# Optimization experiments

Measured on AMD Instinct MI355X. Metric: run time of the kernel, lower is better.

The kernel has to match this reference:

```python
import jax, jax.numpy as jnp
import numpy as np

B = 256        # graph pairs
MAX_SET = 64   # nodes per graph == max_set_size (padding is identity)
E = 512        # edges per graph
D = 128        # node_state_dim == av.filters_3
T = 64         # av.transform_dim
N_PROP = 5
N_TIME = 3
TEMP = 0.1
SINK_ITERS = 20
NG = 2 * B
N = NG * MAX_SET
TOT_E = NG * E


def sinkhorn(log_alpha):
    la = log_alpha / TEMP
    for _ in range(SINK_ITERS):
        la = la - jax.nn.logsumexp(la, axis=2, keepdims=True)
        la = la - jax.nn.logsumexp(la, axis=1, keepdims=True)
    return jnp.exp(la)


def setup_inputs() -> dict:
    key = jax.random.key(0)
    ks = jax.random.split(key, 32)

    def lin(k, i, o):
        return jax.random.normal(k, (i, o), jnp.float32) / np.sqrt(i).astype(np.float32)

    node_features = jax.random.normal(ks[0], (N, 32), jnp.float32)
    edge_features = jax.random.normal(ks[1], (TOT_E, 16), jnp.float32)
    offs = jnp.repeat(jnp.arange(NG, dtype=jnp.int32) * MAX_SET, E)
    from_idx = jax.random.randint(ks[2], (TOT_E,), 0, MAX_SET, jnp.int32) + offs
    to_idx = jax.random.randint(ks[3], (TOT_E,), 0, MAX_SET, jnp.int32) + offs
    return {
        "node_features": node_features, "edge_features": edge_features,
        "from_idx": from_idx, "to_idx": to_idx,
        "node_enc_w": lin(ks[4], 32, D), "node_enc_b": jnp.zeros((D,), jnp.float32),
        "edge_enc_w": lin(ks[5], 16, 64), "edge_enc_b": jnp.zeros((64,), jnp.float32),
        "mw1": lin(ks[6], 2 * D + 64, 2 * D), "mb1": jnp.zeros((2 * D,), jnp.float32),
        "mw2": lin(ks[7], 2 * D, D), "mb2": jnp.zeros((D,), jnp.float32),
        "nw1": lin(ks[8], 2 * D, 2 * D), "nb1": jnp.zeros((2 * D,), jnp.float32),
        "nw2": lin(ks[9], 2 * D, D), "nb2": jnp.zeros((D,), jnp.float32),
        "cw1": lin(ks[10], 2 * D, 2 * D), "cb1": jnp.zeros((2 * D,), jnp.float32),
        "cw2": lin(ks[11], 2 * D, D), "cb2": jnp.zeros((D,), jnp.float32),
        "t1w": lin(ks[12], D, T), "t1b": jnp.zeros((T,), jnp.float32),
        "t2w": lin(ks[13], T, T), "t2b": jnp.zeros((T,), jnp.float32),
    }


def reference(node_features, edge_features, from_idx, to_idx,
              node_enc_w, node_enc_b, edge_enc_w, edge_enc_b,
              mw1, mb1, mw2, mb2, nw1, nb1, nw2, nb2,
              cw1, cb1, cw2, cb2, t1w, t1b, t2w, t2b):
    # Encoder (GMN GraphEncoder: linear maps on raw node/edge features)
    h0 = node_features @ node_enc_w + node_enc_b          # [N, D]
    e0 = edge_features @ edge_enc_w + edge_enc_b          # [TOT_E, 64]
    store = jnp.zeros((N, D * (N_PROP + 1)), h0.dtype)    # node_feature_store
    plan = None
    for _t in range(N_TIME):
        h = h0
        parts = [jnp.zeros((N, D), h0.dtype)]             # slot 0 stays zero
        for p in range(1, N_PROP + 1):
            inter = store[:, (p - 1) * D: p * D]          # time_update_idx == 'k_t'
            comb = jax.nn.relu(jnp.concatenate([h, inter], 1) @ cw1 + cb1) @ cw2 + cb2
            # GraphPropLayer: gather -> message MLP -> segment_sum -> node update MLP
            msg_in = jnp.concatenate([comb[from_idx], comb[to_idx], e0], 1)
            messages = jax.nn.relu(msg_in @ mw1 + mb1) @ mw2 + mb2
            agg = jax.ops.segment_sum(messages, to_idx, num_segments=N)
            h = jax.nn.relu(jnp.concatenate([comb, agg], 1) @ nw1 + nb1) @ nw2 + nb2
            parts.append(h)
        store = jnp.concatenate(parts, 1)                 # [N, D*(K+1)]
        # split into padded query/corpus stacks (all graphs have MAX_SET nodes,
        # so F.pad and the size masks are identity here)
        s = store.reshape(NG, MAX_SET, -1)
        q, c = s[0::2], s[1::2]                           # [B, M, D*(K+1)]
        tq = jax.nn.relu(q[:, :, -D:] @ t1w + t1b) @ t2w + t2b
        tc = jax.nn.relu(c[:, :, -D:] @ t1w + t1b) @ t2w + t2b
        sim = jnp.einsum('bqt,bct->bqc', tq, tc)
        plan = sinkhorn(sim)                              # node transport plan [B,M,M]
        qfc = jnp.einsum('bqc,bcd->bqd', plan, c)
        cfq = jnp.einsum('bqc,bqd->bcd', plan, q)
        inter_feats = jnp.stack([qfc, cfq], 1)[:, :, :, D:].reshape(N, N_PROP * D)
        store = store.at[:, D:].set(inter_feats)
    return plan
```

## Files before the change

### kernel.cpp

```cpp
#include <hip/hip_runtime.h>
#include <hip/hip_bf16.h>

#define NNODES   32768
#define NGROUPS  512
#define EPG      512
#define ND       (32768l*128)

typedef __attribute__((ext_vector_type(4))) float f32x4;
typedef __attribute__((ext_vector_type(8))) short bf16x8;

__device__ __forceinline__ short f2bf(float x) {
  unsigned u = __float_as_uint(x);
  unsigned r = (u + 0x7FFF + ((u >> 16) & 1)) >> 16;
  return (short)r;
}
__device__ __forceinline__ float bf2f(short h) {
  return __uint_as_float(((unsigned)(unsigned short)h) << 16);
}
__device__ __forceinline__ void split3(float x, short* ph, short* pm, short* pl, long idx) {
  short h = f2bf(x); float r1 = x - bf2f(h);
  short m = f2bf(r1); float r2 = r1 - bf2f(m);
  ph[idx] = h; pm[idx] = m; pl[idx] = f2bf(r2);
}

__global__ void k_node_enc(const float* __restrict__ nf, const float* __restrict__ w,
                           const float* __restrict__ b, float* __restrict__ h0) {
  int idx = blockIdx.x * 256 + threadIdx.x;
  int row = idx >> 7, col = idx & 127;
  const float* x = nf + row * 32;
  float acc = b[col];
#pragma unroll
  for (int k = 0; k < 32; ++k) acc = fmaf(x[k], w[k * 128 + col], acc);
  h0[idx] = acc;
}

__global__ void k_prep(const float* __restrict__ eew, const float* __restrict__ eeb,
                       const float* __restrict__ mw1, const float* __restrict__ mb1,
                       const float* __restrict__ mb2, const float* __restrict__ nw1,
                       float* __restrict__ Wfold, float* __restrict__ bfold,
                       float* __restrict__ vbias) {
  const int c = threadIdx.x, b = blockIdx.x;
  if (b < 16) {
    float a = 0.f;
    for (int j = 0; j < 64; ++j) a = fmaf(eew[b * 64 + j], mw1[(256 + j) * 256 + c], a);
    Wfold[b * 256 + c] = a;
  } else if (b == 16) {
    float a = mb1[c];
    for (int j = 0; j < 64; ++j) a = fmaf(eeb[j], mw1[(256 + j) * 256 + c], a);
    bfold[c] = a;
  } else {
    float a = 0.f;
    for (int j = 0; j < 128; ++j) a = fmaf(mb2[j], nw1[(128 + j) * 256 + c], a);
    vbias[c] = a;
  }
}

__global__ void k_wsplit3(const float* __restrict__ W, int C, int Kd,
                          short* __restrict__ th, short* __restrict__ tm,
                          short* __restrict__ tl) {
  const int c = blockIdx.x;
  for (int k = threadIdx.x; k < Kd; k += 256) {
    float w = W[(long)k * C + c];
    split3(w, th, tm, tl, c * 256 + k);
  }
}

__global__ void k_csr(const int* __restrict__ from_idx, const int* __restrict__ to_idx,
                      const float* __restrict__ ef,
                      int* __restrict__ csr_f, int* __restrict__ rp_g,
                      float* __restrict__ efp, int* __restrict__ deg) {
  __shared__ int cnt[64], rps[65];
  __shared__ int tls[EPG], fls[EPG];
  __shared__ short ord[EPG];
  const int g = blockIdx.x, tid = threadIdx.x;
  const int be = g * EPG, bn = g * 64;
  if (tid < 64) cnt[tid] = 0;
  __syncthreads();
  for (int e = tid; e < EPG; e += 256) {
    int t = to_idx[be + e] - bn;
    tls[e] = t;
    fls[e] = from_idx[be + e] - bn;
    atomicAdd(&cnt[t], 1);
  }
  __syncthreads();
  if (tid == 0) {
    int s = 0;
    for (int i = 0; i < 64; ++i) { rps[i] = s; s += cnt[i]; }
    rps[64] = s;
  }
  __syncthreads();
  if (tid < 64) {
    int pos = rps[tid];
    for (int e = 0; e < EPG; ++e)
      if (tls[e] == tid) ord[pos++] = (short)e;
  }
  __syncthreads();
  for (int ec = tid; ec < EPG; ec += 256) {
    const int eo = ord[ec];
    csr_f[be + ec] = fls[eo];
    const float4* src = (const float4*)&ef[(long)(be + eo) * 16];
    float4* dst = (float4*)&efp[(long)(be + ec) * 16];
    dst[0] = src[0]; dst[1] = src[1]; dst[2] = src[2]; dst[3] = src[3];
  }
  if (tid < 65) rp_g[g * 65 + tid] = rps[tid];
  if (tid < 64) deg[bn + tid] = cnt[tid];
}

template<int KTOT, bool DEG, bool RPX0, bool WPOUT, bool AGG>
__global__ __launch_bounds__(256, 3)
void k_mlp2m(const float* __restrict__ x0,
             const short* __restrict__ x0h, const short* __restrict__ x0m,
             const short* __restrict__ x0l,
             const float* __restrict__ x1,
             const short* __restrict__ A2h, const short* __restrict__ A2m,
             const short* __restrict__ A2l,
             const short* __restrict__ W1h, const short* __restrict__ W1m,
             const short* __restrict__ W1l,
             const float* __restrict__ b1, const int* __restrict__ deg,
             const float* __restrict__ vbias,
             const short* __restrict__ W2h, const short* __restrict__ W2m,
             const short* __restrict__ W2l,
             const float* __restrict__ b2,
             float* __restrict__ out,
             short* __restrict__ outh, short* __restrict__ outm,
             short* __restrict__ outl) {
  __shared__ short xh[32 * 264];
  __shared__ short xm[32 * 264];
  __shared__ short xl[32 * 264];
  __shared__ int degs[32];
  const int tid = threadIdx.x;
  const long row0 = (long)blockIdx.x * 32;

  const int lane = tid & 63, wid = tid >> 6;
  const int lr = lane & 15;
  const int lk = (lane >> 4) * 8;
  const int rsub = (lane >> 4) * 4;

  if constexpr (AGG) {
    for (int i = tid; i < 2048; i += 256) {
      const int r = i >> 6, q = i & 63;
      float4 v = *(const float4*)&x1[(row0 + r) * 256 + q * 4];
      const int base = r * 264 + q * 4;
      split3(v.x, xh, xm, xl, base + 0);
      split3(v.y, xh, xm, xl, base + 1);
      split3(v.z, xh, xm, xl, base + 2);
      split3(v.w, xh, xm, xl, base + 3);
    }
    __syncthreads();

    f32x4 s0[2][2], s1[2][2];
#pragma unroll
    for (int fc = 0; fc < 2; ++fc)
#pragma unroll
      for (int fr = 0; fr < 2; ++fr) { s0[fr][fc] = {0.f,0.f,0.f,0.f}; s1[fr][fc] = {0.f,0.f,0.f,0.f}; }

#pragma unroll 2
    for (int ks = 0; ks < 4; ++ks) {
      const int k0 = ks * 32 + lk;
      bf16x8 ah[2], am[2], al[2];
#pragma unroll
      for (int fr = 0; fr < 2; ++fr) {
        const int ab = (fr * 16 + lr) * 264 + k0;
        ah[fr] = *(const bf16x8*)&xh[ab];
        am[fr] = *(const bf16x8*)&xm[ab];
        al[fr] = *(const bf16x8*)&xl[ab];
      }
#pragma unroll
      for (int fc = 0; fc < 2; ++fc) {
        const long wrow = (long)(wid * 32 + fc * 16 + lr) * 256 + k0;
        const bf16x8 bh = *(const bf16x8*)&A2h[wrow];
        const bf16x8 bm = *(const bf16x8*)&A2m[wrow];
        const bf16x8 bl = *(const bf16x8*)&A2l[wrow];
#pragma unroll
        for (int fr = 0; fr < 2; ++fr) {
          s0[fr][fc] = __builtin_amdgcn_mfma_f32_16x16x32_bf16(ah[fr], bh, s0[fr][fc], 0, 0, 0);
          s0[fr][fc] = __builtin_amdgcn_mfma_f32_16x16x32_bf16(ah[fr], bm, s0[fr][fc], 0, 0, 0);
          s0[fr][fc] = __builtin_amdgcn_mfma_f32_16x16x32_bf16(am[fr], bh, s0[fr][fc], 0, 0, 0);
          s0[fr][fc] = __builtin_amdgcn_mfma_f32_16x16x32_bf16(ah[fr], bl, s0[fr][fc], 0, 0, 0);
          s0[fr][fc] = __builtin_amdgcn_mfma_f32_16x16x32_bf16(am[fr], bm, s0[fr][fc], 0, 0, 0);
          s0[fr][fc] = __builtin_amdgcn_mfma_f32_16x16x32_bf16(al[fr], bh, s0[fr][fc], 0, 0, 0);
        }
      }
    }
#pragma unroll 2
    for (int ks = 4; ks < 8; ++ks) {
      const int k0 = ks * 32 + lk;
      bf16x8 ah[2], am[2], al[2];
#pragma unroll
      for (int fr = 0; fr < 2; ++fr) {
        const int ab = (fr * 16 + lr) * 264 + k0;
        ah[fr] = *(const bf16x8*)&xh[ab];
        am[fr] = *(const bf16x8*)&xm[ab];
        al[fr] = *(const bf16x8*)&xl[ab];
      }
#pragma unroll
      for (int fc = 0; fc < 2; ++fc) {
        const long wrow = (long)(wid * 32 + fc * 16 + lr) * 256 + k0;
        const bf16x8 bh = *(const bf16x8*)&A2h[wrow];
        const bf16x8 bm = *(const bf16x8*)&A2m[wrow];
        const bf16x8 bl = *(const bf16x8*)&A2l[wrow];
#pragma unroll
        for (int fr = 0; fr < 2; ++fr) {
          s1[fr][fc] = __builtin_amdgcn_mfma_f32_16x16x32_bf16(ah[fr], bh, s1[fr][fc], 0, 0, 0);
          s1[fr][fc] = __builtin_amdgcn_mfma_f32_16x16x32_bf16(ah[fr], bm, s1[fr][fc], 0, 0, 0);
          s1[fr][fc] = __builtin_amdgcn_mfma_f32_16x16x32_bf16(am[fr], bh, s1[fr][fc], 0, 0, 0);
          s1[fr][fc] = __builtin_amdgcn_mfma_f32_16x16x32_bf16(ah[fr], bl, s1[fr][fc], 0, 0, 0);
          s1[fr][fc] = __builtin_amdgcn_mfma_f32_16x16x32_bf16(am[fr], bm, s1[fr][fc], 0, 0, 0);
          s1[fr][fc] = __builtin_amdgcn_mfma_f32_16x16x32_bf16(al[fr], bh, s1[fr][fc], 0, 0, 0);
        }
      }
    }
    __syncthreads();

#pragma unroll
    for (int fr = 0; fr < 2; ++fr)
#pragma unroll
      for (int fc = 0; fc < 2; ++fc) {
        const int col = wid * 32 + fc * 16 + lr;
#pragma unroll
        for (int r = 0; r < 4; ++r) {
          const int row = fr * 16 + rsub + r;
          split3(s0[fr][fc][r] + s1[fr][fc][r], xh, xm, xl, row * 264 + 128 + col);
        }
      }
  }

  if constexpr (RPX0) {
    for (int i = tid; i < 32 * 16; i += 256) {
      const int r = i >> 4, q = i & 15;
      const long gb = (row0 + r) * 128 + q * 8;
      const int lb = r * 264 + q * 8;
      *(bf16x8*)&xh[lb] = *(const bf16x8*)&x0h[gb];
      *(bf16x8*)&xm[lb] = *(const bf16x8*)&x0m[gb];
      *(bf16x8*)&xl[lb] = *(const bf16x8*)&x0l[gb];
    }
  } else {
    for (int i = tid; i < 32 * 32; i += 256) {
      const int r = i >> 5, q = i & 31;
      float4 v = *(const float4*)&x0[(row0 + r) * 128 + q * 4];
      const int base = r * 264 + q * 4;
      split3(v.x, xh, xm, xl, base + 0);
      split3(v.y, xh, xm, xl, base + 1);
      split3(v.z, xh, xm, xl, base + 2);
      split3(v.w, xh, xm, xl, base + 3);
    }
  }
  if constexpr (KTOT == 256 && !AGG) {
    for (int i = tid; i < 32 * 32; i += 256) {
      const int r = i >> 5, q = i & 31;
      float4 v = *(const float4*)&x1[(row0 + r) * 128 + q * 4];
      const int base = r * 264 + 128 + q * 4;
      split3(v.x, xh, xm, xl, base + 0);
      split3(v.y, xh, xm, xl, base + 1);
      split3(v.z, xh, xm, xl, base + 2);
      split3(v.w, xh, xm, xl, base + 3);
    }
  }
  if constexpr (DEG) { if (tid < 32) degs[tid] = deg[row0 + tid]; }
  __syncthreads();

  f32x4 acc[2][4];
#pragma unroll
  for (int fc = 0; fc < 4; ++fc) {
    const int col = wid * 64 + fc * 16 + lr;
    const float bv = b1[col];
#pragma unroll
    for (int fr = 0; fr < 2; ++fr) acc[fr][fc] = {bv, bv, bv, bv};
    if constexpr (DEG) {
      const float vb = vbias[col];
#pragma unroll
      for (int fr = 0; fr < 2; ++fr)
#pragma unroll
        for (int r = 0; r < 4; ++r)
          acc[fr][fc][r] += (float)degs[fr * 16 + rsub + r] * vb;
    }
  }

#pragma unroll 2
  for (int ks = 0; ks < KTOT / 32; ++ks) {
    const int k0 = ks * 32 + lk;
    bf16x8 ah[2], am[2], al[2];
#pragma unroll
    for (int fr = 0; fr < 2; ++fr) {
      const int ab = (fr * 16 + lr) * 264 + k0;
      ah[fr] = *(const bf16x8*)&xh[ab];
      am[fr] = *(const bf16x8*)&xm[ab];
      al[fr] = *(const bf16x8*)&xl[ab];
    }
#pragma unroll
    for (int fc = 0; fc < 4; ++fc) {
      const long wrow = (long)(wid * 64 + fc * 16 + lr) * 256 + k0;
      const bf16x8 bh = *(const bf16x8*)&W1h[wrow];
      const bf16x8 bm = *(const bf16x8*)&W1m[wrow];
      const bf16x8 bl = *(const bf16x8*)&W1l[wrow];
#pragma unroll
      for (int fr = 0; fr < 2; ++fr) {
        acc[fr][fc] = __builtin_amdgcn_mfma_f32_16x16x32_bf16(ah[fr], bh, acc[fr][fc], 0, 0, 0);
        acc[fr][fc] = __builtin_amdgcn_mfma_f32_16x16x32_bf16(ah[fr], bm, acc[fr][fc], 0, 0, 0);
        acc[fr][fc] = __builtin_amdgcn_mfma_f32_16x16x32_bf16(am[fr], bh, acc[fr][fc], 0, 0, 0);
        acc[fr][fc] = __builtin_amdgcn_mfma_f32_16x16x32_bf16(ah[fr], bl, acc[fr][fc], 0, 0, 0);
        acc[fr][fc] = __builtin_amdgcn_mfma_f32_16x16x32_bf16(am[fr], bm, acc[fr][fc], 0, 0, 0);
        acc[fr][fc] = __builtin_amdgcn_mfma_f32_16x16x32_bf16(al[fr], bh, acc[fr][fc], 0, 0, 0);
      }
    }
  }
  __syncthreads();

#pragma unroll
  for (int fr = 0; fr < 2; ++fr)
#pragma unroll
    for (int fc = 0; fc < 4; ++fc) {
      const int col = wid * 64 + fc * 16 + lr;
#pragma unroll
      for (int r = 0; r < 4; ++r) {
        const int row = fr * 16 + rsub + r;
        float v = fmaxf(acc[fr][fc][r], 0.f);
        split3(v, xh, xm, xl, row * 264 + col);
      }
    }
  __syncthreads();

  f32x4 acc2[2][2];
#pragma unroll
  for (int fc = 0; fc < 2; ++fc) {
    const float bv = b2[wid * 32 + fc * 16 + lr];
#pragma unroll
    for (int fr = 0; fr < 2; ++fr) acc2[fr][fc] = {bv, bv, bv, bv};
  }
#pragma unroll 2
  for (int ks = 0; ks < 8; ++ks) {
    const int k0 = ks * 32 + lk;
    bf16x8 ah[2], am[2], al[2];
#pragma unroll
    for (int fr = 0; fr < 2; ++fr) {
      const int ab = (fr * 16 + lr) * 264 + k0;
      ah[fr] = *(const bf16x8*)&xh[ab];
      am[fr] = *(const bf16x8*)&xm[ab];
      al[fr] = *(const bf16x8*)&xl[ab];
    }
#pragma unroll
    for (int fc = 0; fc < 2; ++fc) {
      const long wrow = (long)(wid * 32 + fc * 16 + lr) * 256 + k0;
      const bf16x8 bh = *(const bf16x8*)&W2h[wrow];
      const bf16x8 bm = *(const bf16x8*)&W2m[wrow];
      const bf16x8 bl = *(const bf16x8*)&W2l[wrow];
#pragma unroll
      for (int fr = 0; fr < 2; ++fr) {
        acc2[fr][fc] = __builtin_amdgcn_mfma_f32_16x16x32_bf16(ah[fr], bh, acc2[fr][fc], 0, 0, 0);
        acc2[fr][fc] = __builtin_amdgcn_mfma_f32_16x16x32_bf16(ah[fr], bm, acc2[fr][fc], 0, 0, 0);
        acc2[fr][fc] = __builtin_amdgcn_mfma_f32_16x16x32_bf16(am[fr], bh, acc2[fr][fc], 0, 0, 0);
        acc2[fr][fc] = __builtin_amdgcn_mfma_f32_16x16x32_bf16(ah[fr], bl, acc2[fr][fc], 0, 0, 0);
        acc2[fr][fc] = __builtin_amdgcn_mfma_f32_16x16x32_bf16(am[fr], bm, acc2[fr][fc], 0, 0, 0);
        acc2[fr][fc] = __builtin_amdgcn_mfma_f32_16x16x32_bf16(al[fr], bh, acc2[fr][fc], 0, 0, 0);
      }
    }
  }
#pragma unroll
  for (int fr = 0; fr < 2; ++fr)
#pragma unroll
    for (int fc = 0; fc < 2; ++fc) {
      const int col = wid * 32 + fc * 16 + lr;
#pragma unroll
      for (int r = 0; r < 4; ++r) {
        const long gi = (row0 + fr * 16 + rsub + r) * 128 + col;
        if constexpr (WPOUT) {
          split3(acc2[fr][fc][r], outh, outm, outl, gi);
        } else {
          out[gi] = acc2[fr][fc][r];
        }
      }
    }
}

__global__ __launch_bounds__(256, 3)
void k_edgeb(const short* __restrict__ chp, const short* __restrict__ cmp,
             const short* __restrict__ clp,
             const float* __restrict__ efp,
             const short* __restrict__ m1h, const short* __restrict__ m1m,
             const short* __restrict__ m1l,
             const float* __restrict__ Wfold, const float* __restrict__ bfold,
             const int* __restrict__ csr_f, const int* __restrict__ rp_g,
             float* __restrict__ ag) {
  __shared__ __align__(16) float cAB[2 * 64 * 68];
  __shared__ short fl[EPG];
  __shared__ int rp[65];
  float* cA = cAB;
  float* cB = cAB + 64 * 68;

  const int tid = threadIdx.x;
  const int g = blockIdx.x, cb = blockIdx.y;
  const int be = g * EPG, bn = g * 64;
  const int col0 = cb * 64;

  for (int i = tid; i < EPG; i += 256) fl[i] = (short)csr_f[be + i];
  if (tid < 65) rp[tid] = rp_g[g * 65 + tid];

  const int lane = tid & 63, wid = tid >> 6;
  const int lr = lane & 15;
  const int lk = (lane >> 4) * 8;
  const int rsub = (lane >> 4) * 4;
  const int ng = tid >> 4, cg = tid & 15;
  const int n0 = ng * 4, cq = cg * 4;

  {
    const int isB = wid >> 1;
    const int cw = (wid & 1) * 32;
    const int wkof = isB * 128;
    float* dstC = isB ? cB : cA;
#pragma unroll 1
    for (int hf = 0; hf < 2; ++hf) {
      f32x4 c[2][2];
#pragma unroll
      for (int fr = 0; fr < 2; ++fr)
#pragma unroll
        for (int fc = 0; fc < 2; ++fc) c[fr][fc] = {0.f, 0.f, 0.f, 0.f};
      for (int ks = 0; ks < 4; ++ks) {
        const int k0 = ks * 32 + lk;
        bf16x8 ah[2], am[2], al[2];
#pragma unroll
        for (int fr = 0; fr < 2; ++fr) {
          const long ga = (long)(bn + (hf * 2 + fr) * 16 + lr) * 128 + k0;
          ah[fr] = *(const bf16x8*)&chp[ga];
          am[fr] = *(const bf16x8*)&cmp[ga];
          al[fr] = *(const bf16x8*)&clp[ga];
        }
#pragma unroll
        for (int fc = 0; fc < 2; ++fc) {
          const long wrow = (long)(col0 + cw + fc * 16 + lr) * 256 + wkof + k0;
          const bf16x8 bh = *(const bf16x8*)&m1h[wrow];
          const bf16x8 bm = *(const bf16x8*)&m1m[wrow];
          const bf16x8 bl = *(const bf16x8*)&m1l[wrow];
#pragma unroll
          for (int fr = 0; fr < 2; ++fr) {
            c[fr][fc] = __builtin_amdgcn_mfma_f32_16x16x32_bf16(ah[fr], bh, c[fr][fc], 0, 0, 0);
            c[fr][fc] = __builtin_amdgcn_mfma_f32_16x16x32_bf16(ah[fr], bm, c[fr][fc], 0, 0, 0);
            c[fr][fc] = __builtin_amdgcn_mfma_f32_16x16x32_bf16(am[fr], bh, c[fr][fc], 0, 0, 0);
            c[fr][fc] = __builtin_amdgcn_mfma_f32_16x16x32_bf16(ah[fr], bl, c[fr][fc], 0, 0, 0);
            c[fr][fc] = __builtin_amdgcn_mfma_f32_16x16x32_bf16(am[fr], bm, c[fr][fc], 0, 0, 0);
            c[fr][fc] = __builtin_amdgcn_mfma_f32_16x16x32_bf16(al[fr], bh, c[fr][fc], 0, 0, 0);
          }
        }
      }
#pragma unroll
      for (int fr = 0; fr < 2; ++fr)
#pragma unroll
        for (int fc = 0; fc < 2; ++fc) {
          const int col = cw + fc * 16 + lr;
#pragma unroll
          for (int r = 0; r < 4; ++r)
            dstC[((hf * 2 + fr) * 16 + rsub + r) * 68 + col] = c[fr][fc][r];
        }
    }
  }
  float4 Wf[16];
#pragma unroll
  for (int k = 0; k < 16; ++k) Wf[k] = *(const float4*)&Wfold[k * 256 + col0 + cq];
  const float4 bf = *(const float4*)&bfold[col0 + cq];
  __syncthreads();

#pragma unroll
  for (int i = 0; i < 4; ++i) {
    const int n = n0 + i;
    const float4 cBn = *(const float4*)&cB[n * 68 + cq];
    const int eEnd = rp[n + 1];
    float4 a0 = make_float4(0.f, 0.f, 0.f, 0.f);
    float4 a1 = make_float4(0.f, 0.f, 0.f, 0.f);
    float4 a2 = make_float4(0.f, 0.f, 0.f, 0.f);
    int e = rp[n];
    for (; e + 2 < eEnd; e += 3) {
      const int f0 = fl[e], f1 = fl[e + 1], f2 = fl[e + 2];
      const float* er0 = efp + (long)(be + e) * 16;
      const float* er1 = efp + (long)(be + e + 1) * 16;
      const float* er2 = efp + (long)(be + e + 2) * 16;
      float4 ea[4], eb[4], ec[4];
#pragma unroll
      for (int kq = 0; kq < 4; ++kq) {
        ea[kq] = ((const float4*)er0)[kq];
        eb[kq] = ((const float4*)er1)[kq];
        ec[kq] = ((const float4*)er2)[kq];
      }
      float4 h0 = bf, h1 = bf, h2 = bf;
#pragma unroll
      for (int kq = 0; kq < 4; ++kq) {
        const float ev0[4] = {ea[kq].x, ea[kq].y, ea[kq].z, ea[kq].w};
        const float ev1[4] = {eb[kq].x, eb[kq].y, eb[kq].z, eb[kq].w};
        const float ev2[4] = {ec[kq].x, ec[kq].y, ec[kq].z, ec[kq].w};
#pragma unroll
        for (int s = 0; s < 4; ++s) {
          const float4 w = Wf[kq * 4 + s];
          h0.x = fmaf(ev0[s], w.x, h0.x); h0.y = fmaf(ev0[s], w.y, h0.y);
          h0.z = fmaf(ev0[s], w.z, h0.z); h0.w = fmaf(ev0[s], w.w, h0.w);
          h1.x = fmaf(ev1[s], w.x, h1.x); h1.y = fmaf(ev1[s], w.y, h1.y);
          h1.z = fmaf(ev1[s], w.z, h1.z); h1.w = fmaf(ev1[s], w.w, h1.w);
          h2.x = fmaf(ev2[s], w.x, h2.x); h2.y = fmaf(ev2[s], w.y, h2.y);
          h2.z = fmaf(ev2[s], w.z, h2.z); h2.w = fmaf(ev2[s], w.w, h2.w);
        }
      }
      const float4 va0 = *(const float4*)&cA[f0 * 68 + cq];
      const float4 va1 = *(const float4*)&cA[f1 * 68 + cq];
      const float4 va2 = *(const float4*)&cA[f2 * 68 + cq];
      a0.x += fmaxf(h0.x + va0.x + cBn.x, 0.f);
      a0.y += fmaxf(h0.y + va0.y + cBn.y, 0.f);
      a0.z += fmaxf(h0.z + va0.z + cBn.z, 0.f);
      a0.w += fmaxf(h0.w + va0.w + cBn.w, 0.f);
      a1.x += fmaxf(h1.x + va1.x + cBn.x, 0.f);
      a1.y += fmaxf(h1.y + va1.y + cBn.y, 0.f);
      a1.z += fmaxf(h1.z + va1.z + cBn.z, 0.f);
      a1.w += fmaxf(h1.w + va1.w + cBn.w, 0.f);
      a2.x += fmaxf(h2.x + va2.x + cBn.x, 0.f);
      a2.y += fmaxf(h2.y + va2.y + cBn.y, 0.f);
      a2.z += fmaxf(h2.z + va2.z + cBn.z, 0.f);
      a2.w += fmaxf(h2.w + va2.w + cBn.w, 0.f);
    }
    for (; e < eEnd; ++e) {
      const int f = fl[e];
      const float* er = efp + (long)(be + e) * 16;
      float4 h = bf;
#pragma unroll
      for (int kq = 0; kq < 4; ++kq) {
        const float4 e4 = ((const float4*)er)[kq];
        const float ev[4] = {e4.x, e4.y, e4.z, e4.w};
#pragma unroll
        for (int s = 0; s < 4; ++s) {
          const float4 w = Wf[kq * 4 + s];
          h.x = fmaf(ev[s], w.x, h.x); h.y = fmaf(ev[s], w.y, h.y);
          h.z = fmaf(ev[s], w.z, h.z); h.w = fmaf(ev[s], w.w, h.w);
        }
      }
      const float4 va = *(const float4*)&cA[f * 68 + cq];
      a0.x += fmaxf(h.x + va.x + cBn.x, 0.f);
      a0.y += fmaxf(h.y + va.y + cBn.y, 0.f);
      a0.z += fmaxf(h.z + va.z + cBn.z, 0.f);
      a0.w += fmaxf(h.w + va.w + cBn.w, 0.f);
    }
    a0.x += a1.x; a0.y += a1.y; a0.z += a1.z; a0.w += a1.w;
    a0.x += a2.x; a0.y += a2.y; a0.z += a2.z; a0.w += a2.w;
    *(float4*)&ag[(long)(bn + n) * 256 + col0 + cq] = a0;
  }
}

__global__ void k_tfeat(const float* __restrict__ x,
                        const float* __restrict__ t1w, const float* __restrict__ t1b,
                        const float* __restrict__ t2w, const float* __restrict__ t2b,
                        float* __restrict__ tf) {
  __shared__ float xs[4][128];
  __shared__ float ys[4][64];
  const int tid = threadIdx.x;
  const long row0 = (long)blockIdx.x * 4;
  for (int i = tid; i < 512; i += 256)
    xs[i >> 7][i & 127] = x[(row0 + (i >> 7)) * 128 + (i & 127)];
  __syncthreads();
  const int r = tid >> 6, c = tid & 63;
  float acc = t1b[c];
#pragma unroll 4
  for (int k = 0; k < 128; ++k) acc = fmaf(xs[r][k], t1w[k * 64 + c], acc);
  ys[r][c] = fmaxf(acc, 0.f);
  __syncthreads();
  float a2 = t2b[c];
#pragma unroll 4
  for (int k = 0; k < 64; ++k) a2 = fmaf(ys[r][k], t2w[k * 64 + c], a2);
  tf[(row0 + r) * 64 + c] = a2;
}

__global__ void k_sim(const float* __restrict__ tf, float* __restrict__ sim) {
  const int b = blockIdx.x, tid = threadIdx.x;
  __shared__ float tq[64][65];
  __shared__ float tcs[64][65];
  for (int i = tid; i < 4096; i += 256) {
    tq[i >> 6][i & 63]  = tf[(long)b * 8192 + i];
    tcs[i >> 6][i & 63] = tf[(long)b * 8192 + 4096 + i];
  }
  __syncthreads();
  const int m = tid >> 2, j0 = (tid & 3) * 16;
#pragma unroll
  for (int j = 0; j < 16; ++j) {
    float a = 0.f;
#pragma unroll 4
    for (int k = 0; k < 64; ++k) a = fmaf(tq[m][k], tcs[j0 + j][k], a);
    sim[(long)b * 4096 + m * 64 + j0 + j] = a;
  }
}

__global__ void k_sink(float* __restrict__ sim, float* __restrict__ outp) {
  const int b = blockIdx.x, tid = threadIdx.x;
  __shared__ float la[64][65];
  const float C = 14.426950408889634f;
  for (int i = tid; i < 4096; i += 256)
    la[i >> 6][i & 63] = sim[(long)b * 4096 + i] * C;
  __syncthreads();
  const int r4 = tid >> 2, l4 = tid & 3;
  for (int it = 0; it < 20; ++it) {
    {
      float m = -3.4e38f;
#pragma unroll
      for (int i = 0; i < 16; ++i) m = fmaxf(m, la[r4][l4 + 4 * i]);
      m = fmaxf(m, __shfl_xor(m, 1)); m = fmaxf(m, __shfl_xor(m, 2));
      float s = 0.f;
#pragma unroll
      for (int i = 0; i < 16; ++i) s += exp2f(la[r4][l4 + 4 * i] - m);
      s += __shfl_xor(s, 1); s += __shfl_xor(s, 2);
      const float lse = m + log2f(s);
#pragma unroll
      for (int i = 0; i < 16; ++i) la[r4][l4 + 4 * i] -= lse;
    }
    __syncthreads();
    {
      float m = -3.4e38f;
#pragma unroll
      for (int i = 0; i < 16; ++i) m = fmaxf(m, la[l4 + 4 * i][r4]);
      m = fmaxf(m, __shfl_xor(m, 1)); m = fmaxf(m, __shfl_xor(m, 2));
      float s = 0.f;
#pragma unroll
      for (int i = 0; i < 16; ++i) s += exp2f(la[l4 + 4 * i][r4] - m);
      s += __shfl_xor(s, 1); s += __shfl_xor(s, 2);
      const float lse = m + log2f(s);
#pragma unroll
      for (int i = 0; i < 16; ++i) la[l4 + 4 * i][r4] -= lse;
    }
    __syncthreads();
  }
  for (int i = tid; i < 4096; i += 256) {
    const float v = exp2f(la[i >> 6][i & 63]);
    outp[(long)b * 4096 + i] = v;
    sim[(long)b * 4096 + i] = v;
  }
}

__global__ void k_mix(const float* __restrict__ plan, const float* __restrict__ src,
                      float* __restrict__ dst) {
  const int b = blockIdx.x, tid = threadIdx.x;
  __shared__ float pl[64][65];
  __shared__ float qs[64][128];
  __shared__ float cs[64][128];
  const long qbase = (long)(2 * b) * 64, cbase = qbase + 64;
  for (int i = tid; i < 4096; i += 256) pl[i >> 6][i & 63] = plan[(long)b * 4096 + i];
  for (int i = tid; i < 8192; i += 256) {
    qs[i >> 7][i & 127] = src[qbase * 128 + i];
    cs[i >> 7][i & 127] = src[cbase * 128 + i];
  }
  __syncthreads();
  const int d = tid & 127, m0 = (tid >> 7) * 32;
  for (int m = m0; m < m0 + 32; ++m) {
    float a = 0.f;
#pragma unroll 4
    for (int j = 0; j < 64; ++j) a = fmaf(pl[m][j], cs[j][d], a);
    dst[(qbase + m) * 128 + d] = a;
  }
  for (int j = m0; j < m0 + 32; ++j) {
    float a = 0.f;
#pragma unroll 4
    for (int m = 0; m < 64; ++m) a = fmaf(pl[m][j], qs[m][d], a);
    dst[(cbase + j) * 128 + d] = a;
  }
}

extern "C" void kernel_launch(void* const* d_in, const int* in_sizes, int n_in,
                              void* d_out, int out_size, void* d_ws, size_t ws_size,
                              hipStream_t stream) {
  const float* nf  = (const float*)d_in[0];
  const float* ef  = (const float*)d_in[1];
  const int* from_idx = (const int*)d_in[2];
  const int* to_idx   = (const int*)d_in[3];
  const float* new_w = (const float*)d_in[4];
  const float* new_b = (const float*)d_in[5];
  const float* eew = (const float*)d_in[6];
  const float* eeb = (const float*)d_in[7];
  const float* mw1 = (const float*)d_in[8];
  const float* mb1 = (const float*)d_in[9];
  const float* mw2 = (const float*)d_in[10];
  const float* mb2 = (const float*)d_in[11];
  const float* nw1 = (const float*)d_in[12];
  const float* nb1 = (const float*)d_in[13];
  const float* nw2 = (const float*)d_in[14];
  const float* nb2 = (const float*)d_in[15];
  const float* cw1 = (const float*)d_in[16];
  const float* cb1 = (const float*)d_in[17];
  const float* cw2 = (const float*)d_in[18];
  const float* cb2 = (const float*)d_in[19];
  const float* t1w = (const float*)d_in[20];
  const float* t1b = (const float*)d_in[21];
  const float* t2w = (const float*)d_in[22];
  const float* t2b = (const float*)d_in[23];

  float* W = (float*)d_ws;
  float* h0     = W;
  float* aggM0  = h0 + ND;
  float* ag     = aggM0 + ND;
  float* parts  = ag + 2 * ND;
  float* efp    = parts + 5 * ND;
  float* Wfold  = efp + 262144l * 16;
  float* bfold  = Wfold + 4096;
  float* vbias  = bfold + 256;
  int*   deg    = (int*)(vbias + 256);
  int*   csr_f  = deg + 32768;
  int*   rp_g   = csr_f + 262144;
  short* cw1t_h = (short*)(rp_g + 33280);
  short* cw1t_m = cw1t_h + 65536;
  short* cw1t_l = cw1t_m + 65536;
  short* nw1t_h = cw1t_l + 65536;
  short* nw1t_m = nw1t_h + 65536;
  short* nw1t_l = nw1t_m + 65536;
  short* cw2t_h = nw1t_l + 65536;
  short* cw2t_m = cw2t_h + 32768;
  short* cw2t_l = cw2t_m + 32768;
  short* nw2t_h = cw2t_l + 32768;
  short* nw2t_m = nw2t_h + 32768;
  short* nw2t_l = nw2t_m + 32768;
  short* m1t_h  = nw2t_l + 32768;
  short* m1t_m  = m1t_h + 65536;
  short* m1t_l  = m1t_m + 65536;
  short* m2t_h  = m1t_l + 65536;
  short* m2t_m  = m2t_h + 32768;
  short* m2t_l  = m2t_m + 32768;
  short* chp    = m2t_l + 32768;
  short* cmp    = chp + 32768l * 128;
  short* clp    = cmp + 32768l * 128;
  float* tf     = aggM0;
  float* sim    = aggM0 + 2097152;
  float* outp   = (float*)d_out;

  k_prep<<<18, 256, 0, stream>>>(eew, eeb, mw1, mb1, mb2, nw1, Wfold, bfold, vbias);
  k_csr<<<512, 256, 0, stream>>>(from_idx, to_idx, ef, csr_f, rp_g, efp, deg);
  k_wsplit3<<<256, 256, 0, stream>>>(cw1, 256, 256, cw1t_h, cw1t_m, cw1t_l);
  k_wsplit3<<<256, 256, 0, stream>>>(nw1, 256, 256, nw1t_h, nw1t_m, nw1t_l);
  k_wsplit3<<<128, 256, 0, stream>>>(cw2, 128, 256, cw2t_h, cw2t_m, cw2t_l);
  k_wsplit3<<<128, 256, 0, stream>>>(nw2, 128, 256, nw2t_h, nw2t_m, nw2t_l);
  k_wsplit3<<<256, 256, 0, stream>>>(mw1, 256, 256, m1t_h, m1t_m, m1t_l);
  k_wsplit3<<<128, 256, 0, stream>>>(mw2, 128, 256, m2t_h, m2t_m, m2t_l);
  k_node_enc<<<16384, 256, 0, stream>>>(nf, new_w, new_b, h0);

  for (int t = 0; t < 3; ++t) {
    const float* hprev = h0;
    for (int p = 1; p <= 5; ++p) {
      if (t > 0 && p > 1)
        k_mlp2m<256, false, false, true, false><<<1024, 256, 0, stream>>>(
            hprev, nullptr, nullptr, nullptr,
            parts + (long)(p - 1) * ND, nullptr, nullptr, nullptr,
            cw1t_h, cw1t_m, cw1t_l, cb1, nullptr, nullptr,
            cw2t_h, cw2t_m, cw2t_l, cb2, nullptr, chp, cmp, clp);
      else
        k_mlp2m<128, false, false, true, false><<<1024, 256, 0, stream>>>(
            hprev, nullptr, nullptr, nullptr, nullptr, nullptr, nullptr, nullptr,
            cw1t_h, cw1t_m, cw1t_l, cb1, nullptr, nullptr,
            cw2t_h, cw2t_m, cw2t_l, cb2, nullptr, chp, cmp, clp);
      k_edgeb<<<dim3(512, 4), 256, 0, stream>>>(chp, cmp, clp, efp,
                                                m1t_h, m1t_m, m1t_l,
                                                Wfold, bfold, csr_f, rp_g, ag);
      float* hnew = parts + (long)(p - 1) * ND;
      k_mlp2m<256, true, true, false, true><<<1024, 256, 0, stream>>>(
          nullptr, chp, cmp, clp, ag, m2t_h, m2t_m, m2t_l,
          nw1t_h, nw1t_m, nw1t_l, nb1, deg, vbias,
          nw2t_h, nw2t_m, nw2t_l, nb2, hnew, nullptr, nullptr, nullptr);
      hprev = hnew;
    }
    k_tfeat<<<8192, 256, 0, stream>>>(parts + 4 * ND, t1w, t1b, t2w, t2b, tf);
    k_sim<<<256, 256, 0, stream>>>(tf, sim);
    k_sink<<<256, 256, 0, stream>>>(sim, outp);
    if (t < 2) {
      for (int pi = 3; pi >= 0; --pi)
        k_mix<<<256, 256, 0, stream>>>(sim, parts + (long)pi * ND, parts + (long)(pi + 1) * ND);
    }
  }
}
```

Baseline: 5.539 ms.

## Stream MLP operands from global memory with in-register bf16 split, shrink LDS

The fused two-layer MLP kernel stops staging its inputs into three split-bf16 LDS arrays. Each wave now loads fp32 activations straight from global memory and splits them into high, mid and low bf16 parts in registers right before the MFMAs. Only the intermediate hidden layer and the aggregate go through a single fp32 LDS buffer. This removes one staging pass and a barrier and cuts LDS use, so launch bounds rise to 4 blocks per CU. The cost is redundant global loads and split arithmetic across waves, because each wave re-reads and re-splits the same rows.

```diff
diff --git a/kernel.cpp b/kernel.cpp
--- a/kernel.cpp
+++ b/kernel.cpp
@@ -21,6 +21,16 @@
   short h = f2bf(x); float r1 = x - bf2f(h);
   short m = f2bf(r1); float r2 = r1 - bf2f(m);
   ph[idx] = h; pm[idx] = m; pl[idx] = f2bf(r2);
+}
+__device__ __forceinline__ void split8(const float* __restrict__ p,
+                                       bf16x8& vh, bf16x8& vm, bf16x8& vl) {
+#pragma unroll
+  for (int j = 0; j < 8; ++j) {
+    const float x = p[j];
+    const short h = f2bf(x); const float r1 = x - bf2f(h);
+    const short m = f2bf(r1);
+    vh[j] = h; vm[j] = m; vl[j] = f2bf(r1 - bf2f(m));
+  }
 }
 
 __global__ void k_node_enc(const float* __restrict__ nf, const float* __restrict__ w,
@@ -107,7 +117,7 @@
 }
 
 template<int KTOT, bool DEG, bool RPX0, bool WPOUT, bool AGG>
-__global__ __launch_bounds__(256, 3)
+__global__ __launch_bounds__(256, 4)
 void k_mlp2m(const float* __restrict__ x0,
              const short* __restrict__ x0h, const short* __restrict__ x0m,
              const short* __restrict__ x0l,
@@ -124,30 +134,15 @@
              float* __restrict__ out,
              short* __restrict__ outh, short* __restrict__ outm,
              short* __restrict__ outl) {
-  __shared__ short xh[32 * 264];
-  __shared__ short xm[32 * 264];
-  __shared__ short xl[32 * 264];
-  __shared__ int degs[32];
+  __shared__ float buf[32 * 268];
   const int tid = threadIdx.x;
   const long row0 = (long)blockIdx.x * 32;
-
   const int lane = tid & 63, wid = tid >> 6;
   const int lr = lane & 15;
   const int lk = (lane >> 4) * 8;
   const int rsub = (lane >> 4) * 4;
 
   if constexpr (AGG) {
-    for (int i = tid; i < 2048; i += 256) {
-      const int r = i >> 6, q = i & 63;
-      float4 v = *(const float4*)&x1[(row0 + r) * 256 + q * 4];
-      const int base = r * 264 + q * 4;
-      split3(v.x, xh, xm, xl, base + 0);
-      split3(v.y, xh, xm, xl, base + 1);
-      split3(v.z, xh, xm, xl, base + 2);
-      split3(v.w, xh, xm, xl, base + 3);
-    }
-    __syncthreads();
-
     f32x4 s0[2][2], s1[2][2];
 #pragma unroll
     for (int fc = 0; fc < 2; ++fc)
@@ -159,12 +154,8 @@
       const int k0 = ks * 32 + lk;
       bf16x8 ah[2], am[2], al[2];
 #pragma unroll
-      for (int fr = 0; fr < 2; ++fr) {
-        const int ab = (fr * 16 + lr) * 264 + k0;
-        ah[fr] = *(const bf16x8*)&xh[ab];
-        am[fr] = *(const bf16x8*)&xm[ab];
-        al[fr] = *(const bf16x8*)&xl[ab];
-      }
+      for (int fr = 0; fr < 2; ++fr)
+        split8(&x1[(row0 + fr * 16 + lr) * 256 + k0], ah[fr], am[fr], al[fr]);
 #pragma unroll
       for (int fc = 0; fc < 2; ++fc) {
         const long wrow = (long)(wid * 32 + fc * 16 + lr) * 256 + k0;
@@ -187,12 +178,8 @@
       const int k0 = ks * 32 + lk;
       bf16x8 ah[2], am[2], al[2];
 #pragma unroll
-      for (int fr = 0; fr < 2; ++fr) {
-        const int ab = (fr * 16 + lr) * 264 + k0;
-        ah[fr] = *(const bf16x8*)&xh[ab];
-        am[fr] = *(const bf16x8*)&xm[ab];
-        al[fr] = *(const bf16x8*)&xl[ab];
-      }
+      for (int fr = 0; fr < 2; ++fr)
+        split8(&x1[(row0 + fr * 16 + lr) * 256 + k0], ah[fr], am[fr], al[fr]);
 #pragma unroll
       for (int fc = 0; fc < 2; ++fc) {
         const long wrow = (long)(wid * 32 + fc * 16 + lr) * 256 + k0;
@@ -210,54 +197,17 @@
         }
       }
     }
-    __syncthreads();
-
 #pragma unroll
     for (int fr = 0; fr < 2; ++fr)
 #pragma unroll
       for (int fc = 0; fc < 2; ++fc) {
         const int col = wid * 32 + fc * 16 + lr;
 #pragma unroll
-        for (int r = 0; r < 4; ++r) {
-          const int row = fr * 16 + rsub + r;
-          split3(s0[fr][fc][r] + s1[fr][fc][r], xh, xm, xl, row * 264 + 128 + col);
-        }
-      }
-  }
-
-  if constexpr (RPX0) {
-    for (int i = tid; i < 32 * 16; i += 256) {
-      const int r = i >> 4, q = i & 15;
-      const long gb = (row0 + r) * 128 + q * 8;
-      const int lb = r * 264 + q * 8;
-      *(bf16x8*)&xh[lb] = *(const bf16x8*)&x0h[gb];
-      *(bf16x8*)&xm[lb] = *(const bf16x8*)&x0m[gb];
-      *(bf16x8*)&xl[lb] = *(const bf16x8*)&x0l[gb];
-    }
-  } else {
-    for (int i = tid; i < 32 * 32; i += 256) {
-      const int r = i >> 5, q = i & 31;
-      float4 v = *(const float4*)&x0[(row0 + r) * 128 + q * 4];
-      const int base = r * 264 + q * 4;
-      split3(v.x, xh, xm, xl, base + 0);
-      split3(v.y, xh, xm, xl, base + 1);
-      split3(v.z, xh, xm, xl, base + 2);
-      split3(v.w, xh, xm, xl, base + 3);
-    }
-  }
-  if constexpr (KTOT == 256 && !AGG) {
-    for (int i = tid; i < 32 * 32; i += 256) {
-      const int r = i >> 5, q = i & 31;
-      float4 v = *(const float4*)&x1[(row0 + r) * 128 + q * 4];
-      const int base = r * 264 + 128 + q * 4;
-      split3(v.x, xh, xm, xl, base + 0);
-      split3(v.y, xh, xm, xl, base + 1);
-      split3(v.z, xh, xm, xl, base + 2);
-      split3(v.w, xh, xm, xl, base + 3);
-    }
-  }
-  if constexpr (DEG) { if (tid < 32) degs[tid] = deg[row0 + tid]; }
-  __syncthreads();
+        for (int r = 0; r < 4; ++r)
+          buf[(fr * 16 + rsub + r) * 268 + col] = s0[fr][fc][r] + s1[fr][fc][r];
+      }
+    __syncthreads();
+  }
 
   f32x4 acc[2][4];
 #pragma unroll
@@ -272,20 +222,24 @@
       for (int fr = 0; fr < 2; ++fr)
 #pragma unroll
         for (int r = 0; r < 4; ++r)
-          acc[fr][fc][r] += (float)degs[fr * 16 + rsub + r] * vb;
+          acc[fr][fc][r] += (float)deg[row0 + fr * 16 + rsub + r] * vb;
     }
   }
 
 #pragma unroll 2
-  for (int ks = 0; ks < KTOT / 32; ++ks) {
+  for (int ks = 0; ks < 4; ++ks) {
     const int k0 = ks * 32 + lk;
     bf16x8 ah[2], am[2], al[2];
 #pragma unroll
     for (int fr = 0; fr < 2; ++fr) {
-      const int ab = (fr * 16 + lr) * 264 + k0;
-      ah[fr] = *(const bf16x8*)&xh[ab];
-      am[fr] = *(const bf16x8*)&xm[ab];
-      al[fr] = *(const bf16x8*)&xl[ab];
+      const long gb = (row0 + fr * 16 + lr) * 128 + k0;
+      if constexpr (RPX0) {
+        ah[fr] = *(const bf16x8*)&x0h[gb];
+        am[fr] = *(const bf16x8*)&x0m[gb];
+        al[fr] = *(const bf16x8*)&x0l[gb];
+      } else {
+        split8(&x0[gb], ah[fr], am[fr], al[fr]);
+      }
     }
 #pragma unroll
     for (int fc = 0; fc < 4; ++fc) {
@@ -304,6 +258,38 @@
       }
     }
   }
+  if constexpr (KTOT == 256) {
+#pragma unroll 2
+    for (int ks = 4; ks < 8; ++ks) {
+      const int k0 = ks * 32 + lk;
+      bf16x8 ah[2], am[2], al[2];
+#pragma unroll
+      for (int fr = 0; fr < 2; ++fr) {
+        if constexpr (AGG) {
+          split8(&buf[(fr * 16 + lr) * 268 + (k0 - 128)], ah[fr], am[fr], al[fr]);
+        } else {
+          split8(&x1[(row0 + fr * 16 + lr) * 128 + (k0 - 128)], ah[fr], am[fr], al[fr]);
+        }
+      }
+#pragma unroll
+      for (int fc = 0; fc < 4; ++fc) {
+        const long wrow = (long)(wid * 64 + fc * 16 + lr) * 256 + k0;
+        const bf16x8 bh = *(const bf16x8*)&W1h[wrow];
+        const bf16x8 bm = *(const bf16x8*)&W1m[wrow];
+        const bf16x8 bl = *(const bf16x8*)&W1l[wrow];
+#pragma unroll
+        for (int fr = 0; fr < 2; ++fr) {
+          acc[fr][fc] = __builtin_amdgcn_mfma_f32_16x16x32_bf16(ah[fr], bh, acc[fr][fc], 0, 0, 0);
+          acc[fr][fc] = __builtin_amdgcn_mfma_f32_16x16x32_bf16(ah[fr], bm, acc[fr][fc], 0, 0, 0);
+          acc[fr][fc] = __builtin_amdgcn_mfma_f32_16x16x32_bf16(am[fr], bh, acc[fr][fc], 0, 0, 0);
+          acc[fr][fc] = __builtin_amdgcn_mfma_f32_16x16x32_bf16(ah[fr], bl, acc[fr][fc], 0, 0, 0);
+          acc[fr][fc] = __builtin_amdgcn_mfma_f32_16x16x32_bf16(am[fr], bm, acc[fr][fc], 0, 0, 0);
+          acc[fr][fc] = __builtin_amdgcn_mfma_f32_16x16x32_bf16(al[fr], bh, acc[fr][fc], 0, 0, 0);
+        }
+      }
+    }
+  }
+
   __syncthreads();
 
 #pragma unroll
@@ -312,11 +298,8 @@
     for (int fc = 0; fc < 4; ++fc) {
       const int col = wid * 64 + fc * 16 + lr;
 #pragma unroll
-      for (int r = 0; r < 4; ++r) {
-        const int row = fr * 16 + rsub + r;
-        float v = fmaxf(acc[fr][fc][r], 0.f);
-        split3(v, xh, xm, xl, row * 264 + col);
-      }
+      for (int r = 0; r < 4; ++r)
+        buf[(fr * 16 + rsub + r) * 268 + col] = fmaxf(acc[fr][fc][r], 0.f);
     }
   __syncthreads();
 
@@ -332,12 +315,8 @@
     const int k0 = ks * 32 + lk;
     bf16x8 ah[2], am[2], al[2];
 #pragma unroll
-    for (int fr = 0; fr < 2; ++fr) {
-      const int ab = (fr * 16 + lr) * 264 + k0;
-      ah[fr] = *(const bf16x8*)&xh[ab];
-      am[fr] = *(const bf16x8*)&xm[ab];
-      al[fr] = *(const bf16x8*)&xl[ab];
-    }
+    for (int fr = 0; fr < 2; ++fr)
+      split8(&buf[(fr * 16 + lr) * 268 + k0], ah[fr], am[fr], al[fr]);
 #pragma unroll
     for (int fc = 0; fc < 2; ++fc) {
       const long wrow = (long)(wid * 32 + fc * 16 + lr) * 256 + k0;
```

Result: slower. 5.735 ms (+3.5%).
